# Kernel optimization log

Hardware: AMD Instinct MI355X
Metric: run time of the kernel (lower is better)

The kernel has to match this reference:

```python
import jax, jax.numpy as jnp
import numpy as np

N = 100_000      # nodes
E = 1_600_000    # edges
D = 128          # in_dim == hidden_dim
H = 4            # heads
HD = D // H      # per-head dim = 32
B = 8            # graphs in batch
TD = 128         # time_dim
NEG_SLOPE = 0.2
EPS = 1e-5


def _gelu(v):
    return jax.nn.gelu(v, approximate=False)  # torch default erf-GELU


def _layernorm(v, g, b):
    mu = jnp.mean(v, axis=-1, keepdims=True)
    var = jnp.var(v, axis=-1, keepdims=True)
    return (v - mu) * jax.lax.rsqrt(var + EPS) * g + b


def setup_inputs() -> dict:
    key = jax.random.key(0)
    ks = jax.random.split(key, 24)
    s = 1.0 / np.sqrt(D)
    inp = {
        "x": jax.random.normal(ks[0], (N, D), jnp.float32),
        "src": jax.random.randint(ks[1], (E,), 0, N),
        "dst": jax.random.randint(ks[2], (E,), 0, N),
        "graph_ids": jnp.sort(jax.random.randint(ks[3], (N,), 0, B)),
        "time_emb": jax.random.normal(ks[4], (B, TD), jnp.float32),
        # GATv2 params
        "Wsrc": jax.random.normal(ks[5], (D, D), jnp.float32) * s,
        "bsrc": jnp.zeros((D,), jnp.float32),
        "Wdst": jax.random.normal(ks[6], (D, D), jnp.float32) * s,
        "bdst": jnp.zeros((D,), jnp.float32),
        "attn": jax.random.normal(ks[7], (H, HD), jnp.float32) * (1.0 / np.sqrt(HD)),
        "gat_bias": jnp.zeros((D,), jnp.float32),
        # LayerNorms
        "ln1_g": jnp.ones((D,), jnp.float32), "ln1_b": jnp.zeros((D,), jnp.float32),
        "ln2_g": jnp.ones((D,), jnp.float32), "ln2_b": jnp.zeros((D,), jnp.float32),
        # time MLP
        "tW": jax.random.normal(ks[8], (TD, D), jnp.float32) * (1.0 / np.sqrt(TD)),
        "tb": jnp.zeros((D,), jnp.float32),
        # FFN
        "W1": jax.random.normal(ks[9], (D, 2 * D), jnp.float32) * s,
        "b1": jnp.zeros((2 * D,), jnp.float32),
        "W2": jax.random.normal(ks[10], (2 * D, D), jnp.float32) * (1.0 / np.sqrt(2 * D)),
        "b2": jnp.zeros((D,), jnp.float32),
    }
    return inp


def reference(x, src, dst, graph_ids, time_emb, Wsrc, bsrc, Wdst, bdst, attn,
              gat_bias, ln1_g, ln1_b, ln2_g, ln2_b, tW, tb, W1, b1, W2, b2):
    h = _layernorm(x, ln1_g, ln1_b)                       # [N, D]
    # GATv2Conv (share_weights=False, residual=False, activation=gelu)
    feat_src = (h @ Wsrc + bsrc).reshape(N, H, HD)        # [N, H, HD]
    feat_dst = (h @ Wdst + bdst).reshape(N, H, HD)
    e = feat_src[src] + feat_dst[dst]                     # [E, H, HD]
    e = jnp.where(e > 0, e, NEG_SLOPE * e)                # leaky_relu
    scores = jnp.einsum("ehd,hd->eh", e, attn)            # [E, H]
    # segment softmax over incoming edges of each dst node
    m = jax.ops.segment_max(scores, dst, num_segments=N)  # [N, H]
    ex = jnp.exp(scores - m[dst])
    denom = jax.ops.segment_sum(ex, dst, num_segments=N)  # [N, H]
    alpha = ex / denom[dst]                               # [E, H]
    msg = feat_src[src] * alpha[:, :, None]               # [E, H, HD]
    rst = jax.ops.segment_sum(msg, dst, num_segments=N)   # [N, H, HD]
    rst = _gelu(rst + gat_bias.reshape(H, HD))
    h = rst.reshape(N, D)                                 # flatten(1)
    # ragged time-embedding expand: time_condition[graph_of(node)]
    time_cond = _gelu(time_emb @ tW + tb)                 # [B, D]
    h = h + time_cond[graph_ids]
    h = h + x                                             # proj = Identity (in_dim == hidden_dim)
    h2 = _layernorm(h, ln2_g, ln2_b)
    h2 = _gelu(h2 @ W1 + b1) @ W2 + b2                    # FFN
    return h + h2
```

## Files before the change

kernel.cpp:

```cpp
#include <hip/hip_runtime.h>
#include <hip/hip_bf16.h>


#define RB 16
#define NEG_SLOPE 0.2f
#define LN_EPS 1e-5f

typedef __attribute__((ext_vector_type(8))) short short8v;
typedef __attribute__((ext_vector_type(4))) float floatx4;

__device__ __forceinline__ float gelu_erf(float v) {
    return 0.5f * v * (1.0f + erff(v * 0.70710678118654752f));
}
__device__ __forceinline__ unsigned short f2bf(float f) {
    unsigned int u = __float_as_uint(f);
    u += 0x7fffu + ((u >> 16) & 1u);
    return (unsigned short)(u >> 16);
}
__device__ __forceinline__ float bf2f(unsigned short u) {
    return __uint_as_float(((unsigned int)u) << 16);
}

__global__ __launch_bounds__(256) void pack_w(
    const float* __restrict__ W, unsigned short* __restrict__ P, int K, int C)
{
    int tid = blockIdx.x * 256 + threadIdx.x;
    int total = (K >> 5) * (C >> 4) * 64;
    if (tid >= total) return;
    int lane = tid & 63;
    int f = tid >> 6;
    int nkt = K >> 5;
    int nt = f / nkt, kt = f - nt * nkt;
    int col = nt * 16 + (lane & 15);
    int k0 = kt * 32 + 8 * (lane >> 4);
    short8v v;
    #pragma unroll
    for (int i = 0; i < 8; ++i)
        v[i] = (short)f2bf(W[(size_t)(k0 + i) * C + col]);
    *(short8v*)(P + (size_t)tid * 8) = v;
}

__global__ __launch_bounds__(256) void ln1_dual_gemm(
    const float* __restrict__ x,
    const float* __restrict__ ln_g, const float* __restrict__ ln_b,
    const unsigned short* __restrict__ pWs, const float* __restrict__ bsrc,
    const unsigned short* __restrict__ pWd, const float* __restrict__ bdst,
    unsigned short* __restrict__ fs, float* __restrict__ fd, int nrows)
{
    __shared__ __align__(16) float hs[RB][132];
    __shared__ __align__(16) unsigned short pa[4 * 64 * 8];
    __shared__ float s_mu[RB], s_rs[RB];

    const int tid  = threadIdx.x;
    const int row0 = blockIdx.x * RB;
    const int lane = tid & 63;
    const int w    = tid >> 6;

    #pragma unroll
    for (int i = 0; i < 2; ++i) {
        int f   = tid + i * 256;
        int row = f >> 5;
        int c0  = (f & 31) * 4;
        float4 v = make_float4(0.f, 0.f, 0.f, 0.f);
        if (row0 + row < nrows) v = *(const float4*)(x + (size_t)(row0 + row) * 128 + c0);
        *(float4*)&hs[row][c0] = v;
    }
    __syncthreads();

    {
        const int ln = lane;
        #pragma unroll
        for (int rr = 0; rr < 4; ++rr) {
            int row = w * 4 + rr;
            float v0 = hs[row][ln * 2], v1 = hs[row][ln * 2 + 1];
            float s = v0 + v1, sq = v0 * v0 + v1 * v1;
            #pragma unroll
            for (int m = 32; m; m >>= 1) { s += __shfl_xor(s, m); sq += __shfl_xor(sq, m); }
            if (ln == 0) {
                float mu  = s * (1.0f / 128.0f);
                float var = sq * (1.0f / 128.0f) - mu * mu;
                s_mu[row] = mu;
                s_rs[row] = rsqrtf(var + LN_EPS);
            }
        }
    }
    __syncthreads();

    {
        const int kt  = w;
        const int row = lane & 15;
        const int k0  = kt * 32 + 8 * (lane >> 4);
        float mu = s_mu[row], rs = s_rs[row];
        float4 u  = *(float4*)&hs[row][k0];
        float4 v  = *(float4*)&hs[row][k0 + 4];
        float4 g0 = *(const float4*)&ln_g[k0];
        float4 g1 = *(const float4*)&ln_g[k0 + 4];
        float4 c0 = *(const float4*)&ln_b[k0];
        float4 c1 = *(const float4*)&ln_b[k0 + 4];
        short8v pv;
        pv[0] = (short)f2bf((u.x - mu) * rs * g0.x + c0.x);
        pv[1] = (short)f2bf((u.y - mu) * rs * g0.y + c0.y);
        pv[2] = (short)f2bf((u.z - mu) * rs * g0.z + c0.z);
        pv[3] = (short)f2bf((u.w - mu) * rs * g0.w + c0.w);
        pv[4] = (short)f2bf((v.x - mu) * rs * g1.x + c1.x);
        pv[5] = (short)f2bf((v.y - mu) * rs * g1.y + c1.y);
        pv[6] = (short)f2bf((v.z - mu) * rs * g1.z + c1.z);
        pv[7] = (short)f2bf((v.w - mu) * rs * g1.w + c1.w);
        *(short8v*)&pa[(kt * 64 + lane) * 8] = pv;
    }
    __syncthreads();

    short8v a[4];
    #pragma unroll
    for (int kt = 0; kt < 4; ++kt)
        a[kt] = *(const short8v*)&pa[(kt * 64 + lane) * 8];

    #pragma unroll
    for (int j = 0; j < 2; ++j) {
        const int nt = 2 * w + j;
        floatx4 aS = {0.f, 0.f, 0.f, 0.f};
        floatx4 aD = {0.f, 0.f, 0.f, 0.f};
        #pragma unroll
        for (int kt = 0; kt < 4; ++kt) {
            short8v bS = *(const short8v*)(pWs + (size_t)((nt * 4 + kt) * 64 + lane) * 8);
            aS = __builtin_amdgcn_mfma_f32_16x16x32_bf16(a[kt], bS, aS, 0, 0, 0);
            short8v bD = *(const short8v*)(pWd + (size_t)((nt * 4 + kt) * 64 + lane) * 8);
            aD = __builtin_amdgcn_mfma_f32_16x16x32_bf16(a[kt], bD, aD, 0, 0, 0);
        }
        const int col = nt * 16 + (lane & 15);
        const float bS0 = bsrc[col], bD0 = bdst[col];
        #pragma unroll
        for (int r = 0; r < 4; ++r) {
            int grow = row0 + 4 * (lane >> 4) + r;
            if (grow < nrows) {
                fs[(size_t)grow * 128 + col] = f2bf(aS[r] + bS0);
                fd[(size_t)grow * 128 + col] = aD[r] + bD0;
            }
        }
    }
}

__global__ __launch_bounds__(256) void time_mlp(
    const float* __restrict__ temb, const float* __restrict__ tW,
    const float* __restrict__ tb, float* __restrict__ tc, int B)
{
    __shared__ float te[8 * 128];
    int tid = threadIdx.x;
    for (int i = tid; i < B * 128; i += 256) te[i] = temb[i];
    __syncthreads();
    int c = tid & 127, half = tid >> 7;
    for (int b = half * 4; b < half * 4 + 4; ++b) {
        if (b >= B) break;
        float acc = 0.f;
        for (int k = 0; k < 128; ++k) acc = fmaf(te[b * 128 + k], tW[k * 128 + c], acc);
        tc[b * 128 + c] = gelu_erf(acc + tb[c]);
    }
}

__global__ __launch_bounds__(256) void csr_rank(
    const int* __restrict__ dst, int* __restrict__ deg, int* __restrict__ rank, int E)
{
    int e = blockIdx.x * 256 + threadIdx.x;
    if (e < E) rank[e] = atomicAdd(&deg[dst[e]], 1);
}

__global__ __launch_bounds__(256) void scan_blocks(
    const int* __restrict__ deg, int* __restrict__ rs, int* __restrict__ btot, int N)
{
    __shared__ int wtot[4];
    const int t    = threadIdx.x;
    const int idx  = blockIdx.x * 1024 + t * 4;
    int d0 = 0, d1 = 0, d2 = 0, d3 = 0;
    if (idx + 3 < N) {
        int4 v = *(const int4*)(deg + idx);
        d0 = v.x; d1 = v.y; d2 = v.z; d3 = v.w;
    } else {
        if (idx     < N) d0 = deg[idx];
        if (idx + 1 < N) d1 = deg[idx + 1];
        if (idx + 2 < N) d2 = deg[idx + 2];
        if (idx + 3 < N) d3 = deg[idx + 3];
    }
    const int ts = d0 + d1 + d2 + d3;
    const int lane = t & 63, w = t >> 6;
    int incl = ts;
    #pragma unroll
    for (int m = 1; m < 64; m <<= 1) { int u = __shfl_up(incl, m); if (lane >= m) incl += u; }
    if (lane == 63) wtot[w] = incl;
    __syncthreads();
    int woff = 0;
    #pragma unroll
    for (int i = 0; i < 4; ++i) woff += (i < w) ? wtot[i] : 0;
    const int p = woff + incl - ts;
    if (idx + 3 < N) {
        int4 o;
        o.x = p; o.y = p + d0; o.z = p + d0 + d1; o.w = p + d0 + d1 + d2;
        *(int4*)(rs + idx) = o;
    } else {
        if (idx     < N) rs[idx]     = p;
        if (idx + 1 < N) rs[idx + 1] = p + d0;
        if (idx + 2 < N) rs[idx + 2] = p + d0 + d1;
        if (idx + 3 < N) rs[idx + 3] = p + d0 + d1 + d2;
    }
    if (t == 255) btot[blockIdx.x] = woff + incl;
}

__global__ __launch_bounds__(64) void scan_tops(
    int* __restrict__ btot, int nb, int* __restrict__ rs, int N, int E)
{
    const int lane = threadIdx.x;
    int a0 = (2 * lane     < nb) ? btot[2 * lane]     : 0;
    int a1 = (2 * lane + 1 < nb) ? btot[2 * lane + 1] : 0;
    const int ts = a0 + a1;
    int incl = ts;
    #pragma unroll
    for (int m = 1; m < 64; m <<= 1) { int u = __shfl_up(incl, m); if (lane >= m) incl += u; }
    const int ex = incl - ts;
    if (2 * lane     < nb) btot[2 * lane]     = ex;
    if (2 * lane + 1 < nb) btot[2 * lane + 1] = ex + a0;
    if (lane == 0) rs[N] = E;
}

__global__ __launch_bounds__(256) void scan_add(
    int* __restrict__ rs, const int* __restrict__ btot, int N)
{
    int i = blockIdx.x * 256 + threadIdx.x;
    if (i < N) rs[i] += btot[i >> 10];
}

__global__ __launch_bounds__(256) void csr_fill(
    const int* __restrict__ dst, const int* __restrict__ src,
    const int* __restrict__ rs, const int* __restrict__ rank,
    int* __restrict__ srcSorted, int E)
{
    int e = blockIdx.x * 256 + threadIdx.x;
    if (e < E) srcSorted[rs[dst[e]] + rank[e]] = src[e];
}

__global__ __launch_bounds__(256) void gat_gather(
    const unsigned short* __restrict__ fs, float* __restrict__ fd,
    const float* __restrict__ x,
    const int* __restrict__ srcSorted, const int* __restrict__ rs,
    const float* __restrict__ attn, const float* __restrict__ gat_bias,
    const int* __restrict__ gid, const float* __restrict__ tc, int N)
{
    const int lane = threadIdx.x & 63;
    const int wib  = threadIdx.x >> 6;
    const int n    = blockIdx.x * 4 + wib;
    if (n >= N) return;

    const int g   = lane >> 4;
    const int l16 = lane & 15;
    const int d0  = l16 * 8;

    float c1[8], c2[8], vd[8];
    {
        float4 a0 = *(const float4*)(attn + d0);
        float4 a1 = *(const float4*)(attn + d0 + 4);
        c1[0] = 0.6f * a0.x; c2[0] = 0.4f * a0.x;
        c1[1] = 0.6f * a0.y; c2[1] = 0.4f * a0.y;
        c1[2] = 0.6f * a0.z; c2[2] = 0.4f * a0.z;
        c1[3] = 0.6f * a0.w; c2[3] = 0.4f * a0.w;
        c1[4] = 0.6f * a1.x; c2[4] = 0.4f * a1.x;
        c1[5] = 0.6f * a1.y; c2[5] = 0.4f * a1.y;
        c1[6] = 0.6f * a1.z; c2[6] = 0.4f * a1.z;
        c1[7] = 0.6f * a1.w; c2[7] = 0.4f * a1.w;
        float4 v0 = *(const float4*)(fd + (size_t)n * 128 + d0);
        float4 v1 = *(const float4*)(fd + (size_t)n * 128 + d0 + 4);
        vd[0] = v0.x; vd[1] = v0.y; vd[2] = v0.z; vd[3] = v0.w;
        vd[4] = v1.x; vd[5] = v1.y; vd[6] = v1.z; vd[7] = v1.w;
    }

    const int lo = rs[n], hi = rs[n + 1];
    const int T  = (hi - lo + 3) >> 2;

    float den = 0.f;
    float w[8];
    #pragma unroll
    for (int j = 0; j < 8; ++j) w[j] = 0.f;

    int i = lo + g;
    bool vA = (i < hi);
    int sA = vA ? srcSorted[i] : 0;
    uint4 rA = *(const uint4*)(fs + (size_t)sA * 128 + d0);

    for (int t = 0; t < T; ++t) {
        const int inx = i + 4;
        const bool vB = (inx < hi);
        const int sB = vB ? srcSorted[inx] : 0;
        uint4 rB = *(const uint4*)(fs + (size_t)sB * 128 + d0);

        float v[8];
        v[0] = __uint_as_float(rA.x << 16);
        v[1] = __uint_as_float(rA.x & 0xffff0000u);
        v[2] = __uint_as_float(rA.y << 16);
        v[3] = __uint_as_float(rA.y & 0xffff0000u);
        v[4] = __uint_as_float(rA.z << 16);
        v[5] = __uint_as_float(rA.z & 0xffff0000u);
        v[6] = __uint_as_float(rA.w << 16);
        v[7] = __uint_as_float(rA.w & 0xffff0000u);

        float p = 0.f;
        #pragma unroll
        for (int j = 0; j < 8; ++j) {
            float e = v[j] + vd[j];
            p = fmaf(c1[j], e, p);
            p = fmaf(c2[j], fabsf(e), p);
        }
        p += __shfl_xor(p, 1);
        p += __shfl_xor(p, 2);
        float exv = vA ? __expf(p) : 0.f;
        den += exv;
        #pragma unroll
        for (int j = 0; j < 8; ++j) w[j] = fmaf(exv, v[j], w[j]);

        vA = vB; rA = rB; i = inx;
    }

    den += __shfl_xor(den, 16);
    den += __shfl_xor(den, 32);
    #pragma unroll
    for (int j = 0; j < 8; ++j) {
        w[j] += __shfl_xor(w[j], 16);
        w[j] += __shfl_xor(w[j], 32);
    }

    if (g == 0) {
        const float inv = den > 0.f ? 1.0f / den : 0.f;
        const int gg = gid[n];
        float4 x0 = *(const float4*)(x  + (size_t)n * 128 + d0);
        float4 x1 = *(const float4*)(x  + (size_t)n * 128 + d0 + 4);
        float4 t0 = *(const float4*)(tc + (size_t)gg * 128 + d0);
        float4 t1 = *(const float4*)(tc + (size_t)gg * 128 + d0 + 4);
        float4 g0 = *(const float4*)(gat_bias + d0);
        float4 g1 = *(const float4*)(gat_bias + d0 + 4);
        float4 o0, o1;
        o0.x = gelu_erf(w[0] * inv + g0.x) + t0.x + x0.x;
        o0.y = gelu_erf(w[1] * inv + g0.y) + t0.y + x0.y;
        o0.z = gelu_erf(w[2] * inv + g0.z) + t0.z + x0.z;
        o0.w = gelu_erf(w[3] * inv + g0.w) + t0.w + x0.w;
        o1.x = gelu_erf(w[4] * inv + g1.x) + t1.x + x1.x;
        o1.y = gelu_erf(w[5] * inv + g1.y) + t1.y + x1.y;
        o1.z = gelu_erf(w[6] * inv + g1.z) + t1.z + x1.z;
        o1.w = gelu_erf(w[7] * inv + g1.w) + t1.w + x1.w;
        *(float4*)(fd + (size_t)n * 128 + d0)     = o0;
        *(float4*)(fd + (size_t)n * 128 + d0 + 4) = o1;
    }
}

__global__ __launch_bounds__(256) void combine_ffn(
    const float* __restrict__ hmg,
    const float* __restrict__ ln_g, const float* __restrict__ ln_b,
    const unsigned short* __restrict__ pW1, const float* __restrict__ b1,
    const unsigned short* __restrict__ pW2, const float* __restrict__ b2,
    float* __restrict__ out, int nrows)
{
    __shared__ __align__(16) float hs[RB][132];
    __shared__ __align__(16) unsigned short pa[4 * 64 * 8];
    __shared__ __align__(16) unsigned short a2[RB * 264];
    __shared__ float s_mu[RB], s_rs[RB];

    const int tid  = threadIdx.x;
    const int row0 = blockIdx.x * RB;
    const int lane = tid & 63;
    const int w    = tid >> 6;

    #pragma unroll
    for (int i = 0; i < 2; ++i) {
        int f   = tid + i * 256;
        int row = f >> 5;
        int c0  = (f & 31) * 4;
        float4 v = make_float4(0.f, 0.f, 0.f, 0.f);
        if (row0 + row < nrows) v = *(const float4*)(hmg + (size_t)(row0 + row) * 128 + c0);
        *(float4*)&hs[row][c0] = v;
    }
    __syncthreads();

    {
        const int ln = lane;
        #pragma unroll
        for (int rr = 0; rr < 4; ++rr) {
            int row = w * 4 + rr;
            float v0 = hs[row][ln * 2], v1 = hs[row][ln * 2 + 1];
            float s = v0 + v1, sq = v0 * v0 + v1 * v1;
            #pragma unroll
            for (int m = 32; m; m >>= 1) { s += __shfl_xor(s, m); sq += __shfl_xor(sq, m); }
            if (ln == 0) {
                float mu  = s * (1.0f / 128.0f);
                float var = sq * (1.0f / 128.0f) - mu * mu;
                s_mu[row] = mu;
                s_rs[row] = rsqrtf(var + LN_EPS);
            }
        }
    }
    __syncthreads();

    {
        const int kt  = w;
        const int row = lane & 15;
        const int k0  = kt * 32 + 8 * (lane >> 4);
        float mu = s_mu[row], rs = s_rs[row];
        float4 u  = *(float4*)&hs[row][k0];
        float4 v  = *(float4*)&hs[row][k0 + 4];
        float4 g0 = *(const float4*)&ln_g[k0];
        float4 g1 = *(const float4*)&ln_g[k0 + 4];
        float4 c0 = *(const float4*)&ln_b[k0];
        float4 c1 = *(const float4*)&ln_b[k0 + 4];
        short8v pv;
        pv[0] = (short)f2bf((u.x - mu) * rs * g0.x + c0.x);
        pv[1] = (short)f2bf((u.y - mu) * rs * g0.y + c0.y);
        pv[2] = (short)f2bf((u.z - mu) * rs * g0.z + c0.z);
        pv[3] = (short)f2bf((u.w - mu) * rs * g0.w + c0.w);
        pv[4] = (short)f2bf((v.x - mu) * rs * g1.x + c1.x);
        pv[5] = (short)f2bf((v.y - mu) * rs * g1.y + c1.y);
        pv[6] = (short)f2bf((v.z - mu) * rs * g1.z + c1.z);
        pv[7] = (short)f2bf((v.w - mu) * rs * g1.w + c1.w);
        *(short8v*)&pa[(kt * 64 + lane) * 8] = pv;
    }
    __syncthreads();

    {
        short8v a[4];
        #pragma unroll
        for (int kt = 0; kt < 4; ++kt)
            a[kt] = *(const short8v*)&pa[(kt * 64 + lane) * 8];

        #pragma unroll
        for (int jj = 0; jj < 4; ++jj) {
            const int nt = 4 * w + jj;
            floatx4 acc = {0.f, 0.f, 0.f, 0.f};
            #pragma unroll
            for (int kt = 0; kt < 4; ++kt) {
                short8v b = *(const short8v*)(pW1 + (size_t)((nt * 4 + kt) * 64 + lane) * 8);
                acc = __builtin_amdgcn_mfma_f32_16x16x32_bf16(a[kt], b, acc, 0, 0, 0);
            }
            const int col = nt * 16 + (lane & 15);
            const float bb = b1[col];
            #pragma unroll
            for (int r = 0; r < 4; ++r) {
                int rowD = 4 * (lane >> 4) + r;
                a2[rowD * 264 + col] = f2bf(gelu_erf(acc[r] + bb));
            }
        }
    }
    __syncthreads();

    {
        floatx4 acc2[2] = {{0.f, 0.f, 0.f, 0.f}, {0.f, 0.f, 0.f, 0.f}};
        #pragma unroll
        for (int kt = 0; kt < 8; ++kt) {
            short8v af = *(const short8v*)&a2[(lane & 15) * 264 + kt * 32 + 8 * (lane >> 4)];
            #pragma unroll
            for (int j = 0; j < 2; ++j) {
                const int nt = 2 * w + j;
                short8v b = *(const short8v*)(pW2 + (size_t)((nt * 8 + kt) * 64 + lane) * 8);
                acc2[j] = __builtin_amdgcn_mfma_f32_16x16x32_bf16(af, b, acc2[j], 0, 0, 0);
            }
        }
        #pragma unroll
        for (int j = 0; j < 2; ++j) {
            const int col = (2 * w + j) * 16 + (lane & 15);
            const float bb = b2[col];
            #pragma unroll
            for (int r = 0; r < 4; ++r) {
                int rowD = 4 * (lane >> 4) + r;
                int grow = row0 + rowD;
                if (grow < nrows)
                    out[(size_t)grow * 128 + col] = hs[rowD][col] + acc2[j][r] + bb;
            }
        }
    }
}

extern "C" void kernel_launch(void* const* d_in, const int* in_sizes, int n_in,
                              void* d_out, int out_size, void* d_ws, size_t ws_size,
                              hipStream_t stream)
{
    const float* x    = (const float*)d_in[0];
    const int*   src  = (const int*)  d_in[1];
    const int*   dst  = (const int*)  d_in[2];
    const int*   gid  = (const int*)  d_in[3];
    const float* temb = (const float*)d_in[4];
    const float* Wsrc = (const float*)d_in[5];
    const float* bsrc = (const float*)d_in[6];
    const float* Wdst = (const float*)d_in[7];
    const float* bdst = (const float*)d_in[8];
    const float* attn = (const float*)d_in[9];
    const float* gbias= (const float*)d_in[10];
    const float* ln1g = (const float*)d_in[11];
    const float* ln1b = (const float*)d_in[12];
    const float* ln2g = (const float*)d_in[13];
    const float* ln2b = (const float*)d_in[14];
    const float* tW   = (const float*)d_in[15];
    const float* tb   = (const float*)d_in[16];
    const float* W1   = (const float*)d_in[17];
    const float* b1   = (const float*)d_in[18];
    const float* W2   = (const float*)d_in[19];
    const float* b2   = (const float*)d_in[20];

    const int N = in_sizes[0] / 128;
    const int E = in_sizes[1];
    const int B = in_sizes[4] / 128;
    float* out = (float*)d_out;

    char* ws = (char*)d_ws;
    size_t off = 0;
    auto alloc = [&](size_t bytes) { void* p = ws + off; off += (bytes + 255) & ~(size_t)255; return p; };
    unsigned short* fs  = (unsigned short*)alloc((size_t)N * 128 * 2);
    float* fd           = (float*)         alloc((size_t)N * 128 * 4);
    int*   deg          = (int*)           alloc((size_t)N * 4);
    int*   rsb          = (int*)           alloc((size_t)(N + 1) * 4);
    int*   rank         = (int*)           alloc((size_t)E * 4);
    int*   srcSorted    = (int*)           alloc((size_t)E * 4);
    float* tc           = (float*)         alloc((size_t)B * 128 * 4);
    int*   btot         = (int*)           alloc((size_t)1024 * 4);
    unsigned short* pWs = (unsigned short*)alloc((size_t)128 * 128 * 2);
    unsigned short* pWd = (unsigned short*)alloc((size_t)128 * 128 * 2);
    unsigned short* pW1 = (unsigned short*)alloc((size_t)128 * 256 * 2);
    unsigned short* pW2 = (unsigned short*)alloc((size_t)256 * 128 * 2);

    const int nbScan = (N + 1023) >> 10;

    hipMemsetAsync(deg, 0, (size_t)N * 4, stream);
    time_mlp<<<1, 256, 0, stream>>>(temb, tW, tb, tc, B);
    pack_w<<<(4 * 8 * 64 + 255) / 256, 256, 0, stream>>>(Wsrc, pWs, 128, 128);
    pack_w<<<(4 * 8 * 64 + 255) / 256, 256, 0, stream>>>(Wdst, pWd, 128, 128);
    pack_w<<<(4 * 16 * 64 + 255) / 256, 256, 0, stream>>>(W1, pW1, 128, 256);
    pack_w<<<(8 * 8 * 64 + 255) / 256, 256, 0, stream>>>(W2, pW2, 256, 128);
    csr_rank<<<(E + 255) / 256, 256, 0, stream>>>(dst, deg, rank, E);
    scan_blocks<<<nbScan, 256, 0, stream>>>(deg, rsb, btot, N);
    scan_tops<<<1, 64, 0, stream>>>(btot, nbScan, rsb, N, E);
    scan_add<<<(N + 255) / 256, 256, 0, stream>>>(rsb, btot, N);
    csr_fill<<<(E + 255) / 256, 256, 0, stream>>>(dst, src, rsb, rank, srcSorted, E);
    ln1_dual_gemm<<<(N + RB - 1) / RB, 256, 0, stream>>>(
        x, ln1g, ln1b, pWs, bsrc, pWd, bdst, fs, fd, N);
    gat_gather<<<(N + 3) / 4, 256, 0, stream>>>(
        fs, fd, x, srcSorted, rsb, attn, gbias, gid, tc, N);
    combine_ffn<<<(N + RB - 1) / RB, 256, 0, stream>>>(
        fd, ln2g, ln2b, pW1, b1, pW2, b2, out, N);
}
```

Baseline: 291.2 us.

## Merge prep launches, fuse CSR fill into LN1 GEMM, bf16 fd, packed-fp32 gather

Several small launches (time MLP, four weight packs, deg memset) are folded into one prep kernel, and the CSR fill is merged into the LN1 dual-GEMM launch as extra blocks. The destination features are stored in bf16 instead of fp32, which halves that write and read, and the attention output goes to a separate buffer. The gather inner loop is rewritten with float2 vector FMAs so the compiler can emit packed fp32 math. Together these cut launch overhead and memory traffic, at the cost of lower precision on the destination features.

```diff
diff --git a/kernel.cpp b/kernel.cpp
--- a/kernel.cpp
+++ b/kernel.cpp
@@ -8,6 +8,7 @@
 
 typedef __attribute__((ext_vector_type(8))) short short8v;
 typedef __attribute__((ext_vector_type(4))) float floatx4;
+typedef __attribute__((ext_vector_type(2))) float f32x2;
 
 __device__ __forceinline__ float gelu_erf(float v) {
     return 0.5f * v * (1.0f + erff(v * 0.70710678118654752f));
@@ -17,18 +18,14 @@
     u += 0x7fffu + ((u >> 16) & 1u);
     return (unsigned short)(u >> 16);
 }
-__device__ __forceinline__ float bf2f(unsigned short u) {
-    return __uint_as_float(((unsigned int)u) << 16);
-}
-
-__global__ __launch_bounds__(256) void pack_w(
-    const float* __restrict__ W, unsigned short* __restrict__ P, int K, int C)
-{
-    int tid = blockIdx.x * 256 + threadIdx.x;
+
+__device__ __forceinline__ void pack_region(
+    const float* __restrict__ W, unsigned short* __restrict__ P, int K, int C, int idx)
+{
     int total = (K >> 5) * (C >> 4) * 64;
-    if (tid >= total) return;
-    int lane = tid & 63;
-    int f = tid >> 6;
+    if (idx >= total) return;
+    int lane = idx & 63;
+    int f = idx >> 6;
     int nkt = K >> 5;
     int nt = f / nkt, kt = f - nt * nkt;
     int col = nt * 16 + (lane & 15);
@@ -37,123 +34,49 @@
     #pragma unroll
     for (int i = 0; i < 8; ++i)
         v[i] = (short)f2bf(W[(size_t)(k0 + i) * C + col]);
-    *(short8v*)(P + (size_t)tid * 8) = v;
-}
-
-__global__ __launch_bounds__(256) void ln1_dual_gemm(
-    const float* __restrict__ x,
-    const float* __restrict__ ln_g, const float* __restrict__ ln_b,
-    const unsigned short* __restrict__ pWs, const float* __restrict__ bsrc,
-    const unsigned short* __restrict__ pWd, const float* __restrict__ bdst,
-    unsigned short* __restrict__ fs, float* __restrict__ fd, int nrows)
-{
-    __shared__ __align__(16) float hs[RB][132];
-    __shared__ __align__(16) unsigned short pa[4 * 64 * 8];
-    __shared__ float s_mu[RB], s_rs[RB];
-
-    const int tid  = threadIdx.x;
-    const int row0 = blockIdx.x * RB;
-    const int lane = tid & 63;
-    const int w    = tid >> 6;
-
-    #pragma unroll
-    for (int i = 0; i < 2; ++i) {
-        int f   = tid + i * 256;
-        int row = f >> 5;
-        int c0  = (f & 31) * 4;
-        float4 v = make_float4(0.f, 0.f, 0.f, 0.f);
-        if (row0 + row < nrows) v = *(const float4*)(x + (size_t)(row0 + row) * 128 + c0);
-        *(float4*)&hs[row][c0] = v;
-    }
-    __syncthreads();
-
-    {
-        const int ln = lane;
-        #pragma unroll
-        for (int rr = 0; rr < 4; ++rr) {
-            int row = w * 4 + rr;
-            float v0 = hs[row][ln * 2], v1 = hs[row][ln * 2 + 1];
-            float s = v0 + v1, sq = v0 * v0 + v1 * v1;
-            #pragma unroll
-            for (int m = 32; m; m >>= 1) { s += __shfl_xor(s, m); sq += __shfl_xor(sq, m); }
-            if (ln == 0) {
-                float mu  = s * (1.0f / 128.0f);
-                float var = sq * (1.0f / 128.0f) - mu * mu;
-                s_mu[row] = mu;
-                s_rs[row] = rsqrtf(var + LN_EPS);
-            }
-        }
-    }
-    __syncthreads();
-
-    {
-        const int kt  = w;
-        const int row = lane & 15;
-        const int k0  = kt * 32 + 8 * (lane >> 4);
-        float mu = s_mu[row], rs = s_rs[row];
-        float4 u  = *(float4*)&hs[row][k0];
-        float4 v  = *(float4*)&hs[row][k0 + 4];
-        float4 g0 = *(const float4*)&ln_g[k0];
-        float4 g1 = *(const float4*)&ln_g[k0 + 4];
-        float4 c0 = *(const float4*)&ln_b[k0];
-        float4 c1 = *(const float4*)&ln_b[k0 + 4];
-        short8v pv;
-        pv[0] = (short)f2bf((u.x - mu) * rs * g0.x + c0.x);
-        pv[1] = (short)f2bf((u.y - mu) * rs * g0.y + c0.y);
-        pv[2] = (short)f2bf((u.z - mu) * rs * g0.z + c0.z);
-        pv[3] = (short)f2bf((u.w - mu) * rs * g0.w + c0.w);
-        pv[4] = (short)f2bf((v.x - mu) * rs * g1.x + c1.x);
-        pv[5] = (short)f2bf((v.y - mu) * rs * g1.y + c1.y);
-        pv[6] = (short)f2bf((v.z - mu) * rs * g1.z + c1.z);
-        pv[7] = (short)f2bf((v.w - mu) * rs * g1.w + c1.w);
-        *(short8v*)&pa[(kt * 64 + lane) * 8] = pv;
-    }
-    __syncthreads();
-
-    short8v a[4];
-    #pragma unroll
-    for (int kt = 0; kt < 4; ++kt)
-        a[kt] = *(const short8v*)&pa[(kt * 64 + lane) * 8];
-
-    #pragma unroll
-    for (int j = 0; j < 2; ++j) {
-        const int nt = 2 * w + j;
-        floatx4 aS = {0.f, 0.f, 0.f, 0.f};
-        floatx4 aD = {0.f, 0.f, 0.f, 0.f};
-        #pragma unroll
-        for (int kt = 0; kt < 4; ++kt) {
-            short8v bS = *(const short8v*)(pWs + (size_t)((nt * 4 + kt) * 64 + lane) * 8);
-            aS = __builtin_amdgcn_mfma_f32_16x16x32_bf16(a[kt], bS, aS, 0, 0, 0);
-            short8v bD = *(const short8v*)(pWd + (size_t)((nt * 4 + kt) * 64 + lane) * 8);
-            aD = __builtin_amdgcn_mfma_f32_16x16x32_bf16(a[kt], bD, aD, 0, 0, 0);
-        }
-        const int col = nt * 16 + (lane & 15);
-        const float bS0 = bsrc[col], bD0 = bdst[col];
-        #pragma unroll
-        for (int r = 0; r < 4; ++r) {
-            int grow = row0 + 4 * (lane >> 4) + r;
-            if (grow < nrows) {
-                fs[(size_t)grow * 128 + col] = f2bf(aS[r] + bS0);
-                fd[(size_t)grow * 128 + col] = aD[r] + bD0;
-            }
-        }
-    }
-}
-
-__global__ __launch_bounds__(256) void time_mlp(
+    *(short8v*)(P + (size_t)idx * 8) = v;
+}
+
+__global__ __launch_bounds__(256) void prep(
     const float* __restrict__ temb, const float* __restrict__ tW,
-    const float* __restrict__ tb, float* __restrict__ tc, int B)
-{
-    __shared__ float te[8 * 128];
-    int tid = threadIdx.x;
-    for (int i = tid; i < B * 128; i += 256) te[i] = temb[i];
-    __syncthreads();
-    int c = tid & 127, half = tid >> 7;
-    for (int b = half * 4; b < half * 4 + 4; ++b) {
-        if (b >= B) break;
-        float acc = 0.f;
-        for (int k = 0; k < 128; ++k) acc = fmaf(te[b * 128 + k], tW[k * 128 + c], acc);
-        tc[b * 128 + c] = gelu_erf(acc + tb[c]);
+    const float* __restrict__ tb, float* __restrict__ tc, int B,
+    const float* __restrict__ Wsrc, unsigned short* __restrict__ pWs,
+    const float* __restrict__ Wdst, unsigned short* __restrict__ pWd,
+    const float* __restrict__ W1,   unsigned short* __restrict__ pW1,
+    const float* __restrict__ W2,   unsigned short* __restrict__ pW2,
+    int* __restrict__ deg, int N)
+{
+    const int bid = blockIdx.x;
+    const int t   = threadIdx.x;
+    if (bid == 0) {
+        __shared__ float te[8 * 128];
+        for (int i = t; i < B * 128; i += 256) te[i] = temb[i];
+        __syncthreads();
+        int c = t & 127, half = t >> 7;
+        for (int b = half * 4; b < half * 4 + 4; ++b) {
+            if (b >= B) break;
+            float acc = 0.f;
+            for (int k = 0; k < 128; ++k) acc = fmaf(te[b * 128 + k], tW[k * 128 + c], acc);
+            tc[b * 128 + c] = gelu_erf(acc + tb[c]);
+        }
+    } else if (bid < 9) {
+        pack_region(Wsrc, pWs, 128, 128, (bid - 1) * 256 + t);
+    } else if (bid < 17) {
+        pack_region(Wdst, pWd, 128, 128, (bid - 9) * 256 + t);
+    } else if (bid < 33) {
+        pack_region(W1, pW1, 128, 256, (bid - 17) * 256 + t);
+    } else if (bid < 49) {
+        pack_region(W2, pW2, 256, 128, (bid - 33) * 256 + t);
+    } else {
+        int idx = (bid - 49) * 1024 + t * 4;
+        if (idx + 3 < N) {
+            *(int4*)(deg + idx) = make_int4(0, 0, 0, 0);
+        } else {
+            if (idx     < N) deg[idx]     = 0;
+            if (idx + 1 < N) deg[idx + 1] = 0;
+            if (idx + 2 < N) deg[idx + 2] = 0;
+            if (idx + 3 < N) deg[idx + 3] = 0;
+        }
     }
 }
 
@@ -227,18 +150,118 @@
     if (i < N) rs[i] += btot[i >> 10];
 }
 
-__global__ __launch_bounds__(256) void csr_fill(
-    const int* __restrict__ dst, const int* __restrict__ src,
+__global__ __launch_bounds__(256) void ln1_fill(
+    const float* __restrict__ x,
+    const float* __restrict__ ln_g, const float* __restrict__ ln_b,
+    const unsigned short* __restrict__ pWs, const float* __restrict__ bsrc,
+    const unsigned short* __restrict__ pWd, const float* __restrict__ bdst,
+    unsigned short* __restrict__ fs, unsigned short* __restrict__ fdB, int nrows, int nLn1,
+    const int* __restrict__ dst, const int* __restrict__ srcA,
     const int* __restrict__ rs, const int* __restrict__ rank,
     int* __restrict__ srcSorted, int E)
 {
-    int e = blockIdx.x * 256 + threadIdx.x;
-    if (e < E) srcSorted[rs[dst[e]] + rank[e]] = src[e];
+    __shared__ __align__(16) float hs[RB][132];
+    __shared__ __align__(16) unsigned short pa[4 * 64 * 8];
+    __shared__ float s_mu[RB], s_rs[RB];
+
+    if (blockIdx.x >= nLn1) {
+        int e = (blockIdx.x - nLn1) * 256 + threadIdx.x;
+        if (e < E) srcSorted[rs[dst[e]] + rank[e]] = srcA[e];
+        return;
+    }
+
+    const int tid  = threadIdx.x;
+    const int row0 = blockIdx.x * RB;
+    const int lane = tid & 63;
+    const int w    = tid >> 6;
+
+    #pragma unroll
+    for (int i = 0; i < 2; ++i) {
+        int f   = tid + i * 256;
+        int row = f >> 5;
+        int c0  = (f & 31) * 4;
+        float4 v = make_float4(0.f, 0.f, 0.f, 0.f);
+        if (row0 + row < nrows) v = *(const float4*)(x + (size_t)(row0 + row) * 128 + c0);
+        *(float4*)&hs[row][c0] = v;
+    }
+    __syncthreads();
+
+    {
+        const int ln = lane;
+        #pragma unroll
+        for (int rr = 0; rr < 4; ++rr) {
+            int row = w * 4 + rr;
+            float v0 = hs[row][ln * 2], v1 = hs[row][ln * 2 + 1];
+            float s = v0 + v1, sq = v0 * v0 + v1 * v1;
+            #pragma unroll
+            for (int m = 32; m; m >>= 1) { s += __shfl_xor(s, m); sq += __shfl_xor(sq, m); }
+            if (ln == 0) {
+                float mu  = s * (1.0f / 128.0f);
+                float var = sq * (1.0f / 128.0f) - mu * mu;
+                s_mu[row] = mu;
+                s_rs[row] = rsqrtf(var + LN_EPS);
+            }
+        }
+    }
+    __syncthreads();
+
+    {
+        const int kt  = w;
+        const int row = lane & 15;
+        const int k0  = kt * 32 + 8 * (lane >> 4);
+        float mu = s_mu[row], rs2 = s_rs[row];
+        float4 u  = *(float4*)&hs[row][k0];
+        float4 v  = *(float4*)&hs[row][k0 + 4];
+        float4 g0 = *(const float4*)&ln_g[k0];
+        float4 g1 = *(const float4*)&ln_g[k0 + 4];
+        float4 c0 = *(const float4*)&ln_b[k0];
+        float4 c1 = *(const float4*)&ln_b[k0 + 4];
+        short8v pv;
+        pv[0] = (short)f2bf((u.x - mu) * rs2 * g0.x + c0.x);
+        pv[1] = (short)f2bf((u.y - mu) * rs2 * g0.y + c0.y);
+        pv[2] = (short)f2bf((u.z - mu) * rs2 * g0.z + c0.z);
+        pv[3] = (short)f2bf((u.w - mu) * rs2 * g0.w + c0.w);
+        pv[4] = (short)f2bf((v.x - mu) * rs2 * g1.x + c1.x);
+        pv[5] = (short)f2bf((v.y - mu) * rs2 * g1.y + c1.y);
+        pv[6] = (short)f2bf((v.z - mu) * rs2 * g1.z + c1.z);
+        pv[7] = (short)f2bf((v.w - mu) * rs2 * g1.w + c1.w);
+        *(short8v*)&pa[(kt * 64 + lane) * 8] = pv;
+    }
+    __syncthreads();
+
+    short8v a[4];
+    #pragma unroll
+    for (int kt = 0; kt < 4; ++kt)
+        a[kt] = *(const short8v*)&pa[(kt * 64 + lane) * 8];
+
+    #pragma unroll
+    for (int j = 0; j < 2; ++j) {
+        const int nt = 2 * w + j;
+        floatx4 aS = {0.f, 0.f, 0.f, 0.f};
+        floatx4 aD = {0.f, 0.f, 0.f, 0.f};
+        #pragma unroll
+        for (int kt = 0; kt < 4; ++kt) {
+            short8v bS = *(const short8v*)(pWs + (size_t)((nt * 4 + kt) * 64 + lane) * 8);
+            aS = __builtin_amdgcn_mfma_f32_16x16x32_bf16(a[kt], bS, aS, 0, 0, 0);
+            short8v bD = *(const short8v*)(pWd + (size_t)((nt * 4 + kt) * 64 + lane) * 8);
+            aD = __builtin_amdgcn_mfma_f32_16x16x32_bf16(a[kt], bD, aD, 0, 0, 0);
+        }
+        const int col = nt * 16 + (lane & 15);
+        const float bS0 = bsrc[col], bD0 = bdst[col];
+        #pragma unroll
+        for (int r = 0; r < 4; ++r) {
+            int grow = row0 + 4 * (lane >> 4) + r;
+            if (grow < nrows) {
+                fs [(size_t)grow * 128 + col] = f2bf(aS[r] + bS0);
+                fdB[(size_t)grow * 128 + col] = f2bf(aD[r] + bD0);
+            }
+        }
+    }
 }
 
 __global__ __launch_bounds__(256) void gat_gather(
-    const unsigned short* __restrict__ fs, float* __restrict__ fd,
-    const float* __restrict__ x,
+    const unsigned short* __restrict__ fs, const unsigned short* __restrict__ fdB,
+    float* __restrict__ hm, const float* __restrict__ x,
     const int* __restrict__ srcSorted, const int* __restrict__ rs,
     const float* __restrict__ attn, const float* __restrict__ gat_bias,
     const int* __restrict__ gid, const float* __restrict__ tc, int N)
@@ -252,31 +275,27 @@
     const int l16 = lane & 15;
     const int d0  = l16 * 8;
 
-    float c1[8], c2[8], vd[8];
+    f32x2 c1v[4], c2v[4], vdv[4];
     {
         float4 a0 = *(const float4*)(attn + d0);
         float4 a1 = *(const float4*)(attn + d0 + 4);
-        c1[0] = 0.6f * a0.x; c2[0] = 0.4f * a0.x;
-        c1[1] = 0.6f * a0.y; c2[1] = 0.4f * a0.y;
-        c1[2] = 0.6f * a0.z; c2[2] = 0.4f * a0.z;
-        c1[3] = 0.6f * a0.w; c2[3] = 0.4f * a0.w;
-        c1[4] = 0.6f * a1.x; c2[4] = 0.4f * a1.x;
-        c1[5] = 0.6f * a1.y; c2[5] = 0.4f * a1.y;
-        c1[6] = 0.6f * a1.z; c2[6] = 0.4f * a1.z;
-        c1[7] = 0.6f * a1.w; c2[7] = 0.4f * a1.w;
-        float4 v0 = *(const float4*)(fd + (size_t)n * 128 + d0);
-        float4 v1 = *(const float4*)(fd + (size_t)n * 128 + d0 + 4);
-        vd[0] = v0.x; vd[1] = v0.y; vd[2] = v0.z; vd[3] = v0.w;
-        vd[4] = v1.x; vd[5] = v1.y; vd[6] = v1.z; vd[7] = v1.w;
+        float av[8] = {a0.x, a0.y, a0.z, a0.w, a1.x, a1.y, a1.z, a1.w};
+        uint4 vdu = *(const uint4*)(fdB + (size_t)n * 128 + d0);
+        unsigned int uu[4] = {vdu.x, vdu.y, vdu.z, vdu.w};
+        #pragma unroll
+        for (int j = 0; j < 4; ++j) {
+            c1v[j].x = 0.6f * av[2 * j];     c1v[j].y = 0.6f * av[2 * j + 1];
+            c2v[j].x = 0.4f * av[2 * j];     c2v[j].y = 0.4f * av[2 * j + 1];
+            vdv[j].x = __uint_as_float(uu[j] << 16);
+            vdv[j].y = __uint_as_float(uu[j] & 0xffff0000u);
+        }
     }
 
     const int lo = rs[n], hi = rs[n + 1];
     const int T  = (hi - lo + 3) >> 2;
 
     float den = 0.f;
-    float w[8];
-    #pragma unroll
-    for (int j = 0; j < 8; ++j) w[j] = 0.f;
+    f32x2 wv[4] = {{0.f, 0.f}, {0.f, 0.f}, {0.f, 0.f}, {0.f, 0.f}};
 
     int i = lo + g;
     bool vA = (i < hi);
@@ -289,32 +308,38 @@
         const int sB = vB ? srcSorted[inx] : 0;
         uint4 rB = *(const uint4*)(fs + (size_t)sB * 128 + d0);
 
-        float v[8];
-        v[0] = __uint_as_float(rA.x << 16);
-        v[1] = __uint_as_float(rA.x & 0xffff0000u);
-        v[2] = __uint_as_float(rA.y << 16);
-        v[3] = __uint_as_float(rA.y & 0xffff0000u);
-        v[4] = __uint_as_float(rA.z << 16);
-        v[5] = __uint_as_float(rA.z & 0xffff0000u);
-        v[6] = __uint_as_float(rA.w << 16);
-        v[7] = __uint_as_float(rA.w & 0xffff0000u);
-
-        float p = 0.f;
-        #pragma unroll
-        for (int j = 0; j < 8; ++j) {
-            float e = v[j] + vd[j];
-            p = fmaf(c1[j], e, p);
-            p = fmaf(c2[j], fabsf(e), p);
-        }
+        unsigned int ru[4] = {rA.x, rA.y, rA.z, rA.w};
+        f32x2 v2[4];
+        #pragma unroll
+        for (int j = 0; j < 4; ++j) {
+            v2[j].x = __uint_as_float(ru[j] << 16);
+            v2[j].y = __uint_as_float(ru[j] & 0xffff0000u);
+        }
+
+        f32x2 p2 = {0.f, 0.f};
+        #pragma unroll
+        for (int j = 0; j < 4; ++j) {
+            f32x2 e = v2[j] + vdv[j];
+            p2 = __builtin_elementwise_fma(c1v[j], e, p2);
+            p2 = __builtin_elementwise_fma(c2v[j],
+                     __builtin_elementwise_abs(e), p2);
+        }
+        float p = p2.x + p2.y;
         p += __shfl_xor(p, 1);
         p += __shfl_xor(p, 2);
         float exv = vA ? __expf(p) : 0.f;
         den += exv;
-        #pragma unroll
-        for (int j = 0; j < 8; ++j) w[j] = fmaf(exv, v[j], w[j]);
+        f32x2 ex2; ex2.x = exv; ex2.y = exv;
+        #pragma unroll
+        for (int j = 0; j < 4; ++j)
+            wv[j] = __builtin_elementwise_fma(ex2, v2[j], wv[j]);
 
         vA = vB; rA = rB; i = inx;
     }
+
+    float w[8];
+    #pragma unroll
+    for (int j = 0; j < 4; ++j) { w[2 * j] = wv[j].x; w[2 * j + 1] = wv[j].y; }
 
     den += __shfl_xor(den, 16);
     den += __shfl_xor(den, 32);
@@ -342,8 +367,8 @@
         o1.y = gelu_erf(w[5] * inv + g1.y) + t1.y + x1.y;
         o1.z = gelu_erf(w[6] * inv + g1.z) + t1.z + x1.z;
         o1.w = gelu_erf(w[7] * inv + g1.w) + t1.w + x1.w;
-        *(float4*)(fd + (size_t)n * 128 + d0)     = o0;
-        *(float4*)(fd + (size_t)n * 128 + d0 + 4) = o1;
+        *(float4*)(hm + (size_t)n * 128 + d0)     = o0;
+        *(float4*)(hm + (size_t)n * 128 + d0 + 4) = o1;
     }
 }
 
@@ -398,7 +423,7 @@
         const int kt  = w;
         const int row = lane & 15;
         const int k0  = kt * 32 + 8 * (lane >> 4);
-        float mu = s_mu[row], rs = s_rs[row];
+        float mu = s_mu[row], rs2 = s_rs[row];
         float4 u  = *(float4*)&hs[row][k0];
         float4 v  = *(float4*)&hs[row][k0 + 4];
         float4 g0 = *(const float4*)&ln_g[k0];
@@ -406,14 +431,14 @@
         float4 c0 = *(const float4*)&ln_b[k0];
         float4 c1 = *(const float4*)&ln_b[k0 + 4];
         short8v pv;
-        pv[0] = (short)f2bf((u.x - mu) * rs * g0.x + c0.x);
-        pv[1] = (short)f2bf((u.y - mu) * rs * g0.y + c0.y);
-        pv[2] = (short)f2bf((u.z - mu) * rs * g0.z + c0.z);
-        pv[3] = (short)f2bf((u.w - mu) * rs * g0.w + c0.w);
-        pv[4] = (short)f2bf((v.x - mu) * rs * g1.x + c1.x);
-        pv[5] = (short)f2bf((v.y - mu) * rs * g1.y + c1.y);
-        pv[6] = (short)f2bf((v.z - mu) * rs * g1.z + c1.z);
-        pv[7] = (short)f2bf((v.w - mu) * rs * g1.w + c1.w);
+        pv[0] = (short)f2bf((u.x - mu) * rs2 * g0.x + c0.x);
+        pv[1] = (short)f2bf((u.y - mu) * rs2 * g0.y + c0.y);
+        pv[2] = (short)f2bf((u.z - mu) * rs2 * g0.z + c0.z);
+        pv[3] = (short)f2bf((u.w - mu) * rs2 * g0.w + c0.w);
+        pv[4] = (short)f2bf((v.x - mu) * rs2 * g1.x + c1.x);
+        pv[5] = (short)f2bf((v.y - mu) * rs2 * g1.y + c1.y);
+        pv[6] = (short)f2bf((v.z - mu) * rs2 * g1.z + c1.z);
+        pv[7] = (short)f2bf((v.w - mu) * rs2 * g1.w + c1.w);
         *(short8v*)&pa[(kt * 64 + lane) * 8] = pv;
     }
     __syncthreads();
@@ -506,7 +531,8 @@
     size_t off = 0;
     auto alloc = [&](size_t bytes) { void* p = ws + off; off += (bytes + 255) & ~(size_t)255; return p; };
     unsigned short* fs  = (unsigned short*)alloc((size_t)N * 128 * 2);
-    float* fd           = (float*)         alloc((size_t)N * 128 * 4);
+    unsigned short* fdB = (unsigned short*)alloc((size_t)N * 128 * 2);
+    float* hm           = (float*)         alloc((size_t)N * 128 * 4);
     int*   deg          = (int*)           alloc((size_t)N * 4);
     int*   rsb          = (int*)           alloc((size_t)(N + 1) * 4);
     int*   rank         = (int*)           alloc((size_t)E * 4);
@@ -519,22 +545,21 @@
     unsigned short* pW2 = (unsigned short*)alloc((size_t)256 * 128 * 2);
 
     const int nbScan = (N + 1023) >> 10;
-
-    hipMemsetAsync(deg, 0, (size_t)N * 4, stream);
-    time_mlp<<<1, 256, 0, stream>>>(temb, tW, tb, tc, B);
-    pack_w<<<(4 * 8 * 64 + 255) / 256, 256, 0, stream>>>(Wsrc, pWs, 128, 128);
-    pack_w<<<(4 * 8 * 64 + 255) / 256, 256, 0, stream>>>(Wdst, pWd, 128, 128);
-    pack_w<<<(4 * 16 * 64 + 255) / 256, 256, 0, stream>>>(W1, pW1, 128, 256);
-    pack_w<<<(8 * 8 * 64 + 255) / 256, 256, 0, stream>>>(W2, pW2, 256, 128);
+    const int nbZero = (N + 1023) >> 10;
+    const int nLn1   = (N + RB - 1) / RB;
+    const int nFill  = (E + 255) / 256;
+
+    prep<<<49 + nbZero, 256, 0, stream>>>(temb, tW, tb, tc, B,
+        Wsrc, pWs, Wdst, pWd, W1, pW1, W2, pW2, deg, N);
     csr_rank<<<(E + 255) / 256, 256, 0, stream>>>(dst, deg, rank, E);
     scan_blocks<<<nbScan, 256, 0, stream>>>(deg, rsb, btot, N);
     scan_tops<<<1, 64, 0, stream>>>(btot, nbScan, rsb, N, E);
     scan_add<<<(N + 255) / 256, 256, 0, stream>>>(rsb, btot, N);
-    csr_fill<<<(E + 255) / 256, 256, 0, stream>>>(dst, src, rsb, rank, srcSorted, E);
-    ln1_dual_gemm<<<(N + RB - 1) / RB, 256, 0, stream>>>(
-        x, ln1g, ln1b, pWs, bsrc, pWd, bdst, fs, fd, N);
+    ln1_fill<<<nLn1 + nFill, 256, 0, stream>>>(
+        x, ln1g, ln1b, pWs, bsrc, pWd, bdst, fs, fdB, N, nLn1,
+        dst, src, rsb, rank, srcSorted, E);
     gat_gather<<<(N + 3) / 4, 256, 0, stream>>>(
-        fs, fd, x, srcSorted, rsb, attn, gbias, gid, tc, N);
+        fs, fdB, hm, x, srcSorted, rsb, attn, gbias, gid, tc, N);
     combine_ffn<<<(N + RB - 1) / RB, 256, 0, stream>>>(
-        fd, ln2g, ln2b, pW1, b1, pW2, b2, out, N);
-}
+        hm, ln2g, ln2b, pW1, b1, pW2, b2, out, N);
+}
```

Result: faster. 270.0 us (-7.3%).
